# Performance work log

Hardware: AMD Instinct MI355X
Metric: run time of the kernel (lower is better)

Reference implementation:

```python
import jax, jax.numpy as jnp
import numpy as np

NUM_CLASSES = 1000
FEAT_DIM = 128
BATCH = 2048
ALPHA = 1.0


def setup_inputs() -> dict:
    key = jax.random.key(0)
    k1, k2, k3 = jax.random.split(key, 3)
    feat = jax.random.normal(k1, (BATCH, FEAT_DIM), dtype=jnp.float32)
    label = jax.random.randint(k2, (BATCH,), 0, NUM_CLASSES, dtype=jnp.int64)
    # centers ~ kaiming_uniform_(a=sqrt(5)) on a (C, D) matrix -> U(-b, b), b = sqrt(6/((1+5)*D)) = 1/sqrt(D)
    bound = 1.0 / np.sqrt(FEAT_DIM)
    centers = jax.random.uniform(k3, (NUM_CLASSES, FEAT_DIM), dtype=jnp.float32,
                                 minval=-bound, maxval=bound)
    return {"feat": feat, "label": label, "centers": centers}


def reference(feat, label, centers):
    # feat: [B, D], centers: [C, D], label: [B]
    batch_size = feat.shape[0]
    # squared euclidean distance to every center: [B, C]
    diff = feat[:, None, :] - centers[None, :, :]          # [B, C, D]
    dist = jnp.sum(diff * diff, axis=-1)                   # [B, C]
    # margin scaling: multiply true-class distance by (1 + alpha)
    y_onehot = jax.nn.one_hot(label, centers.shape[0], dtype=dist.dtype) * ALPHA + 1.0
    margin_dist = dist * y_onehot
    margin_logits = -0.5 * margin_dist
    logits = -0.5 * dist
    # likelihood regularizer: mean of half squared distance to own center
    cdiff = feat - centers[label]                          # [B, D]
    likelihood = (1.0 / batch_size) * jnp.sum(cdiff * cdiff) / 2.0
    return logits, margin_logits, likelihood
```

## Files before the change

kernel.cpp:

```cpp
#include <hip/hip_runtime.h>
#include <hip/hip_bf16.h>

#define BATCH 2048
#define NCLS  1000
#define FEAT  128

typedef short bf16x8 __attribute__((ext_vector_type(8)));
typedef float f32x16 __attribute__((ext_vector_type(16)));

#define WS_LP   0
#define WS_FN   512
#define WS_CN   2560
#define WS_FB   4096
#define WS_CB   135168

__device__ inline unsigned int f2bf(float f) {
    unsigned int u;
    __builtin_memcpy(&u, &f, 4);
    return (u + 0x7fffu + ((u >> 16) & 1u)) >> 16;
}

__global__ __launch_bounds__(256) void prep_kernel(
    const float* __restrict__ feat,
    const float* __restrict__ centers,
    const int* __restrict__ label,
    float* __restrict__ ws)
{
    __shared__ float lp[4];
    int w    = blockIdx.x * 4 + (threadIdx.x >> 6);
    int lane = threadIdx.x & 63;
    float* fn = ws + WS_FN;
    float* cn = ws + WS_CN;
    unsigned int* fb = (unsigned int*)(ws + WS_FB);
    unsigned int* cb = (unsigned int*)(ws + WS_CB);

    if (w < BATCH) {
        int b = w;
        float2 f = *(const float2*)(feat + b * FEAT + lane * 2);
        int lb = label[b];
        float2 c = *(const float2*)(centers + lb * FEAT + lane * 2);
        fb[b * 64 + lane] = f2bf(f.x) | (f2bf(f.y) << 16);
        float fs = f.x * f.x + f.y * f.y;
        float d0 = f.x - c.x, d1 = f.y - c.y;
        float ls = d0 * d0 + d1 * d1;
        #pragma unroll
        for (int off = 32; off > 0; off >>= 1) {
            fs += __shfl_down(fs, off, 64);
            ls += __shfl_down(ls, off, 64);
        }
        if (lane == 0) {
            fn[b] = fs;
            lp[threadIdx.x >> 6] = ls;
        }
    } else if (w < BATCH + NCLS) {
        int c = w - BATCH;
        float2 cv = *(const float2*)(centers + c * FEAT + lane * 2);
        cb[c * 64 + lane] = f2bf(cv.x) | (f2bf(cv.y) << 16);
        float cs = cv.x * cv.x + cv.y * cv.y;
        #pragma unroll
        for (int off = 32; off > 0; off >>= 1) cs += __shfl_down(cs, off, 64);
        if (lane == 0) cn[c] = cs;
    }

    if (blockIdx.x < 512) {
        __syncthreads();
        if (threadIdx.x == 0)
            ws[WS_LP + blockIdx.x] = lp[0] + lp[1] + lp[2] + lp[3];
    }
}

__global__ __launch_bounds__(256) void lgm_main_kernel(
    const int* __restrict__ label,
    const float* __restrict__ ws,
    float* __restrict__ out)
{
    const float* fn = ws + WS_FN;
    const float* cn = ws + WS_CN;
    const unsigned short* fb = (const unsigned short*)(ws + WS_FB);
    const unsigned short* cb = (const unsigned short*)(ws + WS_CB);

    int tid     = threadIdx.x;
    int lane    = tid & 63;
    int wave    = tid >> 6;
    int tileCol = blockIdx.x & 15;
    int tileRow = blockIdx.x >> 4;
    int rowBase = tileRow * 64 + (wave & 1) * 32;
    int colBase = tileCol * 64 + (wave >> 1) * 32;
    int m       = lane & 31;
    int half    = lane >> 5;

    int r  = rowBase + m;
    int c0 = colBase + m;
    int c  = (c0 < NCLS) ? c0 : (NCLS - 1);

    const unsigned short* ap = fb + r * FEAT + half * 8;
    const unsigned short* bp = cb + c * FEAT + half * 8;

    f32x16 acc = {};
    #pragma unroll
    for (int kk = 0; kk < 8; kk++) {
        bf16x8 a = *(const bf16x8*)(ap + kk * 16);
        bf16x8 b = *(const bf16x8*)(bp + kk * 16);
        acc = __builtin_amdgcn_mfma_f32_32x32x16_bf16(a, b, acc, 0, 0, 0);
    }

    float* out0 = out;
    float* out1 = out + BATCH * NCLS;
    float cnv = cn[c];
    bool  colOK = (c0 < NCLS);
    #pragma unroll
    for (int reg = 0; reg < 16; reg++) {
        int row = rowBase + (reg & 3) + 8 * (reg >> 2) + 4 * half;
        if (colOK) {
            float dist  = fn[row] + cnv - 2.0f * acc[reg];
            float logit = -0.5f * dist;
            int idx = row * NCLS + c0;
            out0[idx] = logit;
            out1[idx] = (c0 == label[row]) ? 2.0f * logit : logit;
        }
    }

    if (blockIdx.x == 0 && tid < 64) {
        float s = 0.0f;
        #pragma unroll
        for (int j = 0; j < 8; j++) s += ws[WS_LP + lane + 64 * j];
        #pragma unroll
        for (int off = 32; off > 0; off >>= 1) s += __shfl_down(s, off, 64);
        if (lane == 0) out[2 * BATCH * NCLS] = s * (0.5f / (float)BATCH);
    }
}

extern "C" void kernel_launch(void* const* d_in, const int* in_sizes, int n_in,
                              void* d_out, int out_size, void* d_ws, size_t ws_size,
                              hipStream_t stream) {
    const float* feat    = (const float*)d_in[0];
    const int*   label   = (const int*)d_in[1];
    const float* centers = (const float*)d_in[2];
    float* ws = (float*)d_ws;

    prep_kernel<<<762, 256, 0, stream>>>(feat, centers, label, ws);
    lgm_main_kernel<<<512, 256, 0, stream>>>(label, ws, (float*)d_out);
}
```

Measured before the change: 71.63 us.

## Fuse prep and GEMM into one kernel with LDS staging and last-block reduction

Merges the prep pass into the main kernel. Each block loads its fp32 feat and center tiles, computes squared norms, converts to bf16 in LDS, runs the MFMA tile, and folds the likelihood term out of the diagonal distances. A global atomic counter lets the last block reduce the per-block partials, and a memset resets the counter each launch. This removes the intermediate workspace round trip and one kernel launch, at the cost of redundant fp32 loads per block. The likelihood now comes from bf16 GEMM distances, so it may be less precise.

```diff
diff --git a/kernel.cpp b/kernel.cpp
--- a/kernel.cpp
+++ b/kernel.cpp
@@ -4,97 +4,86 @@
 #define BATCH 2048
 #define NCLS  1000
 #define FEAT  128
+#define NBLK  512
+#define LDS_STRIDE 136
 
-typedef short bf16x8 __attribute__((ext_vector_type(8)));
-typedef float f32x16 __attribute__((ext_vector_type(16)));
+typedef short  bf16x8 __attribute__((ext_vector_type(8)));
+typedef short  short8 __attribute__((ext_vector_type(8)));
+typedef float  f32x4  __attribute__((ext_vector_type(4)));
+typedef float  f32x16 __attribute__((ext_vector_type(16)));
 
-#define WS_LP   0
-#define WS_FN   512
-#define WS_CN   2560
-#define WS_FB   4096
-#define WS_CB   135168
+#define WS_LP 64
 
-__device__ inline unsigned int f2bf(float f) {
-    unsigned int u;
-    __builtin_memcpy(&u, &f, 4);
-    return (u + 0x7fffu + ((u >> 16) & 1u)) >> 16;
+__device__ inline unsigned int pk2(float x, float y) {
+    __hip_bfloat162 h = __float22bfloat162_rn(make_float2(x, y));
+    unsigned int u; __builtin_memcpy(&u, &h, 4); return u;
 }
 
-__global__ __launch_bounds__(256) void prep_kernel(
+__global__ __launch_bounds__(256) void lgm_fused(
     const float* __restrict__ feat,
     const float* __restrict__ centers,
     const int* __restrict__ label,
-    float* __restrict__ ws)
-{
-    __shared__ float lp[4];
-    int w    = blockIdx.x * 4 + (threadIdx.x >> 6);
-    int lane = threadIdx.x & 63;
-    float* fn = ws + WS_FN;
-    float* cn = ws + WS_CN;
-    unsigned int* fb = (unsigned int*)(ws + WS_FB);
-    unsigned int* cb = (unsigned int*)(ws + WS_CB);
-
-    if (w < BATCH) {
-        int b = w;
-        float2 f = *(const float2*)(feat + b * FEAT + lane * 2);
-        int lb = label[b];
-        float2 c = *(const float2*)(centers + lb * FEAT + lane * 2);
-        fb[b * 64 + lane] = f2bf(f.x) | (f2bf(f.y) << 16);
-        float fs = f.x * f.x + f.y * f.y;
-        float d0 = f.x - c.x, d1 = f.y - c.y;
-        float ls = d0 * d0 + d1 * d1;
-        #pragma unroll
-        for (int off = 32; off > 0; off >>= 1) {
-            fs += __shfl_down(fs, off, 64);
-            ls += __shfl_down(ls, off, 64);
-        }
-        if (lane == 0) {
-            fn[b] = fs;
-            lp[threadIdx.x >> 6] = ls;
-        }
-    } else if (w < BATCH + NCLS) {
-        int c = w - BATCH;
-        float2 cv = *(const float2*)(centers + c * FEAT + lane * 2);
-        cb[c * 64 + lane] = f2bf(cv.x) | (f2bf(cv.y) << 16);
-        float cs = cv.x * cv.x + cv.y * cv.y;
-        #pragma unroll
-        for (int off = 32; off > 0; off >>= 1) cs += __shfl_down(cs, off, 64);
-        if (lane == 0) cn[c] = cs;
-    }
-
-    if (blockIdx.x < 512) {
-        __syncthreads();
-        if (threadIdx.x == 0)
-            ws[WS_LP + blockIdx.x] = lp[0] + lp[1] + lp[2] + lp[3];
-    }
-}
-
-__global__ __launch_bounds__(256) void lgm_main_kernel(
-    const int* __restrict__ label,
-    const float* __restrict__ ws,
+    float* __restrict__ ws,
     float* __restrict__ out)
 {
-    const float* fn = ws + WS_FN;
-    const float* cn = ws + WS_CN;
-    const unsigned short* fb = (const unsigned short*)(ws + WS_FB);
-    const unsigned short* cb = (const unsigned short*)(ws + WS_CB);
+    __shared__ short As[64 * LDS_STRIDE];
+    __shared__ short Bs[64 * LDS_STRIDE];
+    __shared__ float fnp[1024];
+    __shared__ float cnp[1024];
+    __shared__ float fn[64], cn[64];
+    __shared__ int   lab[64];
+    __shared__ float lkp[4];
+    __shared__ float red[256];
+    __shared__ int   isLast;
 
-    int tid     = threadIdx.x;
-    int lane    = tid & 63;
-    int wave    = tid >> 6;
+    int t       = threadIdx.x;
     int tileCol = blockIdx.x & 15;
     int tileRow = blockIdx.x >> 4;
-    int rowBase = tileRow * 64 + (wave & 1) * 32;
-    int colBase = tileCol * 64 + (wave >> 1) * 32;
-    int m       = lane & 31;
-    int half    = lane >> 5;
+    int rowBase = tileRow * 64;
+    int colBase = tileCol * 64;
 
-    int r  = rowBase + m;
-    int c0 = colBase + m;
-    int c  = (c0 < NCLS) ? c0 : (NCLS - 1);
+    #pragma unroll
+    for (int j = 0; j < 4; j++) {
+        int o  = j * 256 + t;
+        int r  = o >> 4;
+        int cc = (o & 15) * 8;
 
-    const unsigned short* ap = fb + r * FEAT + half * 8;
-    const unsigned short* bp = cb + c * FEAT + half * 8;
+        const float* pa = feat + (rowBase + r) * FEAT + cc;
+        f32x4 a0 = *(const f32x4*)pa, a1 = *(const f32x4*)(pa + 4);
+        fnp[(o & 15) * 64 + r] = a0[0]*a0[0] + a0[1]*a0[1] + a0[2]*a0[2] + a0[3]*a0[3]
+                               + a1[0]*a1[0] + a1[1]*a1[1] + a1[2]*a1[2] + a1[3]*a1[3];
+        union { unsigned int u[4]; short8 s; } pa8;
+        pa8.u[0] = pk2(a0[0], a0[1]); pa8.u[1] = pk2(a0[2], a0[3]);
+        pa8.u[2] = pk2(a1[0], a1[1]); pa8.u[3] = pk2(a1[2], a1[3]);
+        *(short8*)(As + r * LDS_STRIDE + cc) = pa8.s;
+
+        int gcol = colBase + r;
+        gcol = (gcol < NCLS) ? gcol : (NCLS - 1);
+        const float* pb = centers + gcol * FEAT + cc;
+        f32x4 b0 = *(const f32x4*)pb, b1 = *(const f32x4*)(pb + 4);
+        cnp[(o & 15) * 64 + r] = b0[0]*b0[0] + b0[1]*b0[1] + b0[2]*b0[2] + b0[3]*b0[3]
+                               + b1[0]*b1[0] + b1[1]*b1[1] + b1[2]*b1[2] + b1[3]*b1[3];
+        union { unsigned int u[4]; short8 s; } pb8;
+        pb8.u[0] = pk2(b0[0], b0[1]); pb8.u[1] = pk2(b0[2], b0[3]);
+        pb8.u[2] = pk2(b1[0], b1[1]); pb8.u[3] = pk2(b1[2], b1[3]);
+        *(short8*)(Bs + r * LDS_STRIDE + cc) = pb8.s;
+    }
+    if (t < 64) lab[t] = label[rowBase + t];
+    __syncthreads();
+    if (t < 64) {
+        float s0 = 0.f, s1 = 0.f;
+        #pragma unroll
+        for (int j = 0; j < 16; j++) { s0 += fnp[j * 64 + t]; s1 += cnp[j * 64 + t]; }
+        fn[t] = s0; cn[t] = s1;
+    }
+    __syncthreads();
+
+    int lane = t & 63, wave = t >> 6;
+    int m    = lane & 31, half = lane >> 5;
+    int rOff = (wave & 1) * 32;
+    int cOff = (wave >> 1) * 32;
+    const short* ap = As + (rOff + m) * LDS_STRIDE + half * 8;
+    const short* bp = Bs + (cOff + m) * LDS_STRIDE + half * 8;
 
     f32x16 acc = {};
     #pragma unroll
@@ -106,27 +95,48 @@
 
     float* out0 = out;
     float* out1 = out + BATCH * NCLS;
-    float cnv = cn[c];
+    int   c0    = colBase + cOff + m;
     bool  colOK = (c0 < NCLS);
+    float cnv   = cn[cOff + m];
+    float lk    = 0.f;
     #pragma unroll
     for (int reg = 0; reg < 16; reg++) {
-        int row = rowBase + (reg & 3) + 8 * (reg >> 2) + 4 * half;
+        int rl    = rOff + (reg & 3) + 8 * (reg >> 2) + 4 * half;
+        float dist  = fn[rl] + cnv - 2.0f * acc[reg];
+        float logit = -0.5f * dist;
         if (colOK) {
-            float dist  = fn[row] + cnv - 2.0f * acc[reg];
-            float logit = -0.5f * dist;
-            int idx = row * NCLS + c0;
+            int idx = (rowBase + rl) * NCLS + c0;
+            bool tru = (c0 == lab[rl]);
             out0[idx] = logit;
-            out1[idx] = (c0 == label[row]) ? 2.0f * logit : logit;
+            out1[idx] = tru ? 2.0f * logit : logit;
+            if (tru) lk += dist;
         }
     }
+    #pragma unroll
+    for (int off = 32; off > 0; off >>= 1) lk += __shfl_down(lk, off, 64);
+    if (lane == 0) lkp[wave] = lk;
+    __syncthreads();
 
-    if (blockIdx.x == 0 && tid < 64) {
-        float s = 0.0f;
-        #pragma unroll
-        for (int j = 0; j < 8; j++) s += ws[WS_LP + lane + 64 * j];
-        #pragma unroll
-        for (int off = 32; off > 0; off >>= 1) s += __shfl_down(s, off, 64);
-        if (lane == 0) out[2 * BATCH * NCLS] = s * (0.5f / (float)BATCH);
+    if (t == 0) {
+        float partial = lkp[0] + lkp[1] + lkp[2] + lkp[3];
+        atomicExch(&ws[WS_LP + blockIdx.x], partial);
+        __threadfence();
+        unsigned int old = atomicAdd((unsigned int*)ws, 1u);
+        isLast = (old == NBLK - 1);
+    }
+    __syncthreads();
+
+    if (isLast) {
+        float v = atomicAdd(&ws[WS_LP + 2 * t], 0.0f)
+                + atomicAdd(&ws[WS_LP + 2 * t + 1], 0.0f);
+        red[t] = v;
+        __syncthreads();
+        if (t < 64) {
+            float s = red[t] + red[t + 64] + red[t + 128] + red[t + 192];
+            #pragma unroll
+            for (int off = 32; off > 0; off >>= 1) s += __shfl_down(s, off, 64);
+            if (t == 0) out[2 * BATCH * NCLS] = s * (0.5f / (float)BATCH);
+        }
     }
 }
 
@@ -138,6 +148,6 @@
     const float* centers = (const float*)d_in[2];
     float* ws = (float*)d_ws;
 
-    prep_kernel<<<762, 256, 0, stream>>>(feat, centers, label, ws);
-    lgm_main_kernel<<<512, 256, 0, stream>>>(label, ws, (float*)d_out);
+    hipMemsetAsync(d_ws, 0, 4, stream);
+    lgm_fused<<<NBLK, 256, 0, stream>>>(feat, centers, label, ws, (float*)d_out);
 }
```

Result: slower. 86.11 us (+20.2%).
